# Kernel optimization log

Measured on AMD Instinct MI355X. Metric: run time of the kernel, lower is better.

Reference implementation:

```python
import jax, jax.numpy as jnp
import numpy as np


def _maxpool2x2(t):
    # t: [B, C, H, W] -> [B, C, H//2, W//2]
    B, C, H, W = t.shape
    return t.reshape(B, C, H // 2, 2, W // 2, 2).max(axis=(3, 5))


def setup_inputs() -> dict:
    key = jax.random.key(0)
    ks = jax.random.split(key, 6)
    ch = 64
    B, H, W = 16, 64, 64
    x = jax.random.normal(ks[0], (B, ch, H, W), dtype=jnp.float32)
    # 1x1 conv weights (spectral-norm wrapper just rescales weights; use unit-scale weights)
    w_theta = jax.random.normal(ks[1], (ch // 8, ch), dtype=jnp.float32) * 0.05
    w_phi = jax.random.normal(ks[2], (ch // 8, ch), dtype=jnp.float32) * 0.05
    w_g = jax.random.normal(ks[3], (ch // 2, ch), dtype=jnp.float32) * 0.05
    w_o = jax.random.normal(ks[4], (ch, ch // 2), dtype=jnp.float32) * 0.05
    gamma = jnp.float32(0.5)  # nonzero so attention branch contributes
    return {"x": x, "w_theta": w_theta, "w_phi": w_phi, "w_g": w_g, "w_o": w_o, "gamma": gamma}


def reference(x, w_theta, w_phi, w_g, w_o, gamma):
    B, C, H, W = x.shape
    N = H * W
    # 1x1 convs are channel contractions
    theta = jnp.einsum('oc,bchw->bohw', w_theta, x).reshape(B, -1, N)          # [B, C/8, N]
    phi = _maxpool2x2(jnp.einsum('oc,bchw->bohw', w_phi, x)).reshape(B, -1, N // 4)  # [B, C/8, N/4]
    g = _maxpool2x2(jnp.einsum('oc,bchw->bohw', w_g, x)).reshape(B, -1, N // 4)      # [B, C/2, N/4]
    # attention: no scaling (faithful to source)
    scores = jnp.einsum('bdn,bdm->bnm', theta, phi)       # [B, N, N/4]
    beta = jax.nn.softmax(scores, axis=-1)
    o = jnp.einsum('bdm,bnm->bdn', g, beta)               # [B, C/2, N]
    o = o.reshape(B, C // 2, H, W)
    o = jnp.einsum('oc,bchw->bohw', w_o, o)               # [B, C, H, W]
    return gamma * o + x
```

## Files before the change

kernel.cpp:

```cpp
#include <hip/hip_runtime.h>

#define BB 16
#define CC 64
#define NN 4096
#define MM 1024

typedef unsigned short u16;
typedef unsigned int u32;
typedef __attribute__((ext_vector_type(8))) short bf16x8;
typedef __attribute__((ext_vector_type(4))) float f32x4;

__device__ inline u16 f2bf(float f) {
    union { float f; u32 u; } v; v.f = f;
    return (u16)((v.u + 0x7FFFu + ((v.u >> 16) & 1u)) >> 16);
}
__device__ inline bf16x8 ld_bf16x8(const u16* p) {
    union { uint4 u; bf16x8 b; } c; c.u = *(const uint4*)p; return c.b;
}
__device__ inline bf16x8 ld2_bf16x8(const u16* p0, const u16* p1) {
    union { uint2 u[2]; bf16x8 b; } c;
    c.u[0] = *(const uint2*)p0;
    c.u[1] = *(const uint2*)p1;
    return c.b;
}
__device__ inline uint2 pack4(u16 a, u16 b, u16 c, u16 d) {
    uint2 r; r.x = (u32)a | ((u32)b << 16); r.y = (u32)c | ((u32)d << 16); return r;
}


__global__ __launch_bounds__(256) void prep_kernel(
    const float* __restrict__ x, const float* __restrict__ w_theta,
    const float* __restrict__ w_phi, const float* __restrict__ w_g,
    u16* __restrict__ theta_b, u16* __restrict__ phi_b, u16* __restrict__ gT_b)
{
    __shared__ float wT[64 * 48];

    const int t = threadIdx.x, w = t >> 6, l = t & 63;
    const int b = blockIdx.y;

    for (int i = t; i < 64 * 8; i += 256)  { int o = i >> 6, c = i & 63; wT[c * 48 + o] = w_theta[i]; }
    for (int i = t; i < 64 * 8; i += 256)  { int o = i >> 6, c = i & 63; wT[c * 48 + 8 + o] = w_phi[i]; }
    for (int i = t; i < 64 * 32; i += 256) { int o = i >> 6, c = i & 63; wT[c * 48 + 16 + o] = w_g[i]; }
    __syncthreads();

    const int nbase = blockIdx.x * 256;
    const float* xb = x + (size_t)b * CC * NN + nbase + 4 * l;

    float acc[12][4];
    #pragma unroll
    for (int k = 0; k < 12; ++k)
        #pragma unroll
        for (int p = 0; p < 4; ++p) acc[k][p] = 0.f;

    #pragma unroll 4
    for (int c = 0; c < 64; ++c) {
        const float4 xv = *(const float4*)(xb + c * NN);
        const float4* wp = (const float4*)(wT + c * 48 + w * 12);
        const float4 wa = wp[0], wb = wp[1], wc = wp[2];
        const float wk[12] = {wa.x, wa.y, wa.z, wa.w, wb.x, wb.y, wb.z, wb.w,
                              wc.x, wc.y, wc.z, wc.w};
        #pragma unroll
        for (int k = 0; k < 12; ++k) {
            acc[k][0] += wk[k] * xv.x; acc[k][1] += wk[k] * xv.y;
            acc[k][2] += wk[k] * xv.z; acc[k][3] += wk[k] * xv.w;
        }
    }

    if (w == 0) {
        #pragma unroll
        for (int p = 0; p < 4; ++p) {
            union { u16 s[8]; uint4 v; } tb;
            #pragma unroll
            for (int k = 0; k < 8; ++k) tb.s[k] = f2bf(acc[k][p]);
            *(uint4*)(theta_b + ((size_t)b * NN + nbase + 4 * l + p) * 8) = tb.v;
        }
    }

    const int start = (w == 0) ? 8 : 0;
    float v0[12], v1[12];
    #pragma unroll
    for (int k = 0; k < 12; ++k) {
        if (k < start) continue;
        float h0 = fmaxf(acc[k][0], acc[k][1]);
        float h1 = fmaxf(acc[k][2], acc[k][3]);
        v0[k] = fmaxf(h0, __shfl_xor(h0, 16, 64));
        v1[k] = fmaxf(h1, __shfl_xor(h1, 16, 64));
    }
    if ((l & 16) == 0) {
        const int prow = l >> 5;
        const int m = (blockIdx.x * 2 + prow) * 32 + 2 * (l & 15);
        #pragma unroll
        for (int k = 0; k < 12; ++k) {
            if (k < start) continue;
            const int kg = w * 12 + k;
            if (kg < 16) {
                phi_b[((size_t)b * MM + m) * 8 + (kg - 8)]     = f2bf(v0[k]);
                phi_b[((size_t)b * MM + m + 1) * 8 + (kg - 8)] = f2bf(v1[k]);
            } else {
                *(u32*)(gT_b + (size_t)b * 32 * MM + (size_t)(kg - 16) * MM + m) =
                    (u32)f2bf(v0[k]) | ((u32)f2bf(v1[k]) << 16);
            }
        }
    }
}

__global__ __launch_bounds__(256, 4) void attn_out_kernel(
    const u16* __restrict__ theta_b, const u16* __restrict__ phi_b,
    const u16* __restrict__ gT_b, const float* __restrict__ w_o,
    const float* __restrict__ x, const float* __restrict__ gamma_p,
    float* __restrict__ out)
{
    __shared__ u16 gs[32 * 136];
    __shared__ u16 oS[64 * 40];

    const int t = threadIdx.x, w = t >> 6, lane = t & 63;
    const int m16 = lane & 15, quad = lane >> 4;
    const int b = blockIdx.y, qbase = blockIdx.x * 64;

    bf16x8 thB = {0, 0, 0, 0, 0, 0, 0, 0};
    if (quad == 0)
        thB = ld_bf16x8(theta_b + ((size_t)b * NN + qbase + w * 16 + m16) * 8);

    bf16x8 woA[4];
    #pragma unroll
    for (int cf = 0; cf < 4; ++cf) {
        const float* wp = w_o + (cf * 16 + m16) * 32 + quad * 8;
        const float4 f0 = *(const float4*)wp;
        const float4 f1 = *(const float4*)(wp + 4);
        bf16x8 a;
        a[0] = f2bf(f0.x); a[1] = f2bf(f0.y); a[2] = f2bf(f0.z); a[3] = f2bf(f0.w);
        a[4] = f2bf(f1.x); a[5] = f2bf(f1.y); a[6] = f2bf(f1.z); a[7] = f2bf(f1.w);
        woA[cf] = a;
    }

    bf16x8 onesA;
    #pragma unroll
    for (int i = 0; i < 8; ++i) onesA[i] = (short)0x3F80;

    const f32x4 zero4 = {0.f, 0.f, 0.f, 0.f};
    f32x4 oT0 = zero4, oT1 = zero4, lacc = zero4;

    const u16* phg = phi_b + (size_t)b * MM * 8;
    const u16* gtg = gT_b + (size_t)b * 32 * MM;

    for (int it = 0; it < 8; ++it) {
        const int keybase = it * 128;
        __syncthreads();
        #pragma unroll
        for (int p2 = 0; p2 < 2; ++p2) {
            const int d = p2 * 16 + (t >> 4);
            const int k0 = (t & 15) * 8;
            *(uint4*)(gs + d * 136 + k0) =
                *(const uint4*)(gtg + (size_t)d * MM + keybase + k0);
        }
        __syncthreads();

        #pragma unroll
        for (int kblk = 0; kblk < 4; ++kblk) {
            bf16x8 phA0 = {0, 0, 0, 0, 0, 0, 0, 0};
            bf16x8 phA1 = {0, 0, 0, 0, 0, 0, 0, 0};
            if (quad == 0) {
                phA0 = ld_bf16x8(phg + (size_t)(keybase + kblk * 32 + m16) * 8);
                phA1 = ld_bf16x8(phg + (size_t)(keybase + kblk * 32 + 16 + m16) * 8);
            }
            const f32x4 Sa = __builtin_amdgcn_mfma_f32_16x16x32_bf16(phA0, thB, zero4, 0, 0, 0);
            const f32x4 Sb = __builtin_amdgcn_mfma_f32_16x16x32_bf16(phA1, thB, zero4, 0, 0, 0);

            bf16x8 pB;
            #pragma unroll
            for (int r = 0; r < 4; ++r) {
                pB[r]     = (short)f2bf(__expf(Sa[r]));
                pB[4 + r] = (short)f2bf(__expf(Sb[r]));
            }

            const u16* g0p = gs + m16 * 136 + kblk * 32 + quad * 4;
            const u16* g1p = gs + (16 + m16) * 136 + kblk * 32 + quad * 4;
            const bf16x8 gA0 = ld2_bf16x8(g0p, g0p + 16);
            const bf16x8 gA1 = ld2_bf16x8(g1p, g1p + 16);

            oT0  = __builtin_amdgcn_mfma_f32_16x16x32_bf16(gA0, pB, oT0, 0, 0, 0);
            oT1  = __builtin_amdgcn_mfma_f32_16x16x32_bf16(gA1, pB, oT1, 0, 0, 0);
            lacc = __builtin_amdgcn_mfma_f32_16x16x32_bf16(onesA, pB, lacc, 0, 0, 0);
        }
    }

    const float inv = 1.0f / lacc[0];
    u16* orow = oS + (w * 16 + m16) * 40;
    *(uint2*)(orow + quad * 4) =
        pack4(f2bf(oT0[0] * inv), f2bf(oT0[1] * inv), f2bf(oT0[2] * inv), f2bf(oT0[3] * inv));
    *(uint2*)(orow + 16 + quad * 4) =
        pack4(f2bf(oT1[0] * inv), f2bf(oT1[1] * inv), f2bf(oT1[2] * inv), f2bf(oT1[3] * inv));
    __syncthreads();

    const bf16x8 oB = ld_bf16x8(oS + (w * 16 + m16) * 40 + quad * 8);
    const float gamma = *gamma_p;
    #pragma unroll
    for (int cf = 0; cf < 4; ++cf) {
        const f32x4 D = __builtin_amdgcn_mfma_f32_16x16x32_bf16(woA[cf], oB, zero4, 0, 0, 0);
        #pragma unroll
        for (int r = 0; r < 4; ++r) {
            const int c = cf * 16 + quad * 4 + r;
            const size_t adr = ((size_t)b * CC + c) * NN + qbase + w * 16 + m16;
            out[adr] = gamma * D[r] + x[adr];
        }
    }
}

extern "C" void kernel_launch(void* const* d_in, const int* in_sizes, int n_in,
                              void* d_out, int out_size, void* d_ws, size_t ws_size,
                              hipStream_t stream) {
    const float* x       = (const float*)d_in[0];
    const float* w_theta = (const float*)d_in[1];
    const float* w_phi   = (const float*)d_in[2];
    const float* w_g     = (const float*)d_in[3];
    const float* w_o     = (const float*)d_in[4];
    const float* gamma   = (const float*)d_in[5];

    u16* theta_b = (u16*)d_ws;
    u16* phi_b   = theta_b + 524288;
    u16* gT_b    = phi_b + 131072;
    float* out   = (float*)d_out;

    prep_kernel<<<dim3(16, 16), 256, 0, stream>>>(x, w_theta, w_phi, w_g,
                                                  theta_b, phi_b, gT_b);
    attn_out_kernel<<<dim3(64, 16), 256, 0, stream>>>(theta_b, phi_b, gT_b,
                                                      w_o, x, gamma, out);
}
```

Before: 120.2 us.

## Restructure prep projection and stage phi/g in LDS with register prefetch

The prep kernel now assigns one pixel per thread and reads weights directly from global memory, computing all 48 output channels. It performs the 2x2 max-pool through a lane shuffle plus an LDS staging buffer instead of the earlier shuffle-only scheme. In the attention kernel, all of phi for the batch is copied into LDS once, and g is processed in 256-key chunks with a register prefetch of the next chunk, halving the number of barriers. Softmax and output bf16 conversion now use the packed bf16 conversion intrinsic. The trade-offs are higher LDS use per block, which may lower occupancy, and more register pressure in prep.

```diff
diff --git a/kernel.cpp b/kernel.cpp
--- a/kernel.cpp
+++ b/kernel.cpp
@@ -1,4 +1,5 @@
 #include <hip/hip_runtime.h>
+#include <hip/hip_bf16.h>
 
 #define BB 16
 #define CC 64
@@ -23,8 +24,9 @@
     c.u[1] = *(const uint2*)p1;
     return c.b;
 }
-__device__ inline uint2 pack4(u16 a, u16 b, u16 c, u16 d) {
-    uint2 r; r.x = (u32)a | ((u32)b << 16); r.y = (u32)c | ((u32)d << 16); return r;
+__device__ inline u32 cvt_pk_bf16(float lo, float hi) {
+    __hip_bfloat162 h = __float22bfloat162_rn(make_float2(lo, hi));
+    return *(u32*)&h;
 }
 
 
@@ -33,74 +35,69 @@
     const float* __restrict__ w_phi, const float* __restrict__ w_g,
     u16* __restrict__ theta_b, u16* __restrict__ phi_b, u16* __restrict__ gT_b)
 {
-    __shared__ float wT[64 * 48];
-
-    const int t = threadIdx.x, w = t >> 6, l = t & 63;
+    __shared__ float pool[40 * 128];
+
+    const int t = threadIdx.x;
     const int b = blockIdx.y;
-
-    for (int i = t; i < 64 * 8; i += 256)  { int o = i >> 6, c = i & 63; wT[c * 48 + o] = w_theta[i]; }
-    for (int i = t; i < 64 * 8; i += 256)  { int o = i >> 6, c = i & 63; wT[c * 48 + 8 + o] = w_phi[i]; }
-    for (int i = t; i < 64 * 32; i += 256) { int o = i >> 6, c = i & 63; wT[c * 48 + 16 + o] = w_g[i]; }
+    const int nbase = blockIdx.x * 256;
+    const int p = nbase + t;
+    const float* xb = x + (size_t)b * CC * NN + p;
+
+    float acc[48];
+    #pragma unroll
+    for (int k = 0; k < 48; ++k) acc[k] = 0.f;
+
+    #pragma unroll 2
+    for (int c4 = 0; c4 < 64; c4 += 4) {
+        const float x0 = xb[(size_t)(c4 + 0) * NN];
+        const float x1 = xb[(size_t)(c4 + 1) * NN];
+        const float x2 = xb[(size_t)(c4 + 2) * NN];
+        const float x3 = xb[(size_t)(c4 + 3) * NN];
+        #pragma unroll
+        for (int k = 0; k < 8; ++k) {
+            const float4 wv = *(const float4*)(w_theta + k * 64 + c4);
+            acc[k] += wv.x * x0 + wv.y * x1 + wv.z * x2 + wv.w * x3;
+        }
+        #pragma unroll
+        for (int k = 0; k < 8; ++k) {
+            const float4 wv = *(const float4*)(w_phi + k * 64 + c4);
+            acc[8 + k] += wv.x * x0 + wv.y * x1 + wv.z * x2 + wv.w * x3;
+        }
+        #pragma unroll
+        for (int k = 0; k < 32; ++k) {
+            const float4 wv = *(const float4*)(w_g + k * 64 + c4);
+            acc[16 + k] += wv.x * x0 + wv.y * x1 + wv.z * x2 + wv.w * x3;
+        }
+    }
+
+    {
+        union { u16 s[8]; uint4 v; } tb;
+        #pragma unroll
+        for (int k = 0; k < 8; ++k) tb.s[k] = f2bf(acc[k]);
+        *(uint4*)(theta_b + ((size_t)b * NN + p) * 8) = tb.v;
+    }
+
+    const int row = t >> 6, col = t & 63;
+    float hv[40];
+    #pragma unroll
+    for (int k = 0; k < 40; ++k) {
+        const float v = acc[8 + k];
+        hv[k] = fmaxf(v, __shfl_xor(v, 1, 64));
+    }
+    if ((col & 1) == 0) {
+        const int pc = col >> 1;
+        #pragma unroll
+        for (int k = 0; k < 40; ++k) pool[k * 128 + row * 32 + pc] = hv[k];
+    }
     __syncthreads();
 
-    const int nbase = blockIdx.x * 256;
-    const float* xb = x + (size_t)b * CC * NN + nbase + 4 * l;
-
-    float acc[12][4];
-    #pragma unroll
-    for (int k = 0; k < 12; ++k)
-        #pragma unroll
-        for (int p = 0; p < 4; ++p) acc[k][p] = 0.f;
-
-    #pragma unroll 4
-    for (int c = 0; c < 64; ++c) {
-        const float4 xv = *(const float4*)(xb + c * NN);
-        const float4* wp = (const float4*)(wT + c * 48 + w * 12);
-        const float4 wa = wp[0], wb = wp[1], wc = wp[2];
-        const float wk[12] = {wa.x, wa.y, wa.z, wa.w, wb.x, wb.y, wb.z, wb.w,
-                              wc.x, wc.y, wc.z, wc.w};
-        #pragma unroll
-        for (int k = 0; k < 12; ++k) {
-            acc[k][0] += wk[k] * xv.x; acc[k][1] += wk[k] * xv.y;
-            acc[k][2] += wk[k] * xv.z; acc[k][3] += wk[k] * xv.w;
-        }
-    }
-
-    if (w == 0) {
-        #pragma unroll
-        for (int p = 0; p < 4; ++p) {
-            union { u16 s[8]; uint4 v; } tb;
-            #pragma unroll
-            for (int k = 0; k < 8; ++k) tb.s[k] = f2bf(acc[k][p]);
-            *(uint4*)(theta_b + ((size_t)b * NN + nbase + 4 * l + p) * 8) = tb.v;
-        }
-    }
-
-    const int start = (w == 0) ? 8 : 0;
-    float v0[12], v1[12];
-    #pragma unroll
-    for (int k = 0; k < 12; ++k) {
-        if (k < start) continue;
-        float h0 = fmaxf(acc[k][0], acc[k][1]);
-        float h1 = fmaxf(acc[k][2], acc[k][3]);
-        v0[k] = fmaxf(h0, __shfl_xor(h0, 16, 64));
-        v1[k] = fmaxf(h1, __shfl_xor(h1, 16, 64));
-    }
-    if ((l & 16) == 0) {
-        const int prow = l >> 5;
-        const int m = (blockIdx.x * 2 + prow) * 32 + 2 * (l & 15);
-        #pragma unroll
-        for (int k = 0; k < 12; ++k) {
-            if (k < start) continue;
-            const int kg = w * 12 + k;
-            if (kg < 16) {
-                phi_b[((size_t)b * MM + m) * 8 + (kg - 8)]     = f2bf(v0[k]);
-                phi_b[((size_t)b * MM + m + 1) * 8 + (kg - 8)] = f2bf(v1[k]);
-            } else {
-                *(u32*)(gT_b + (size_t)b * 32 * MM + (size_t)(kg - 16) * MM + m) =
-                    (u32)f2bf(v0[k]) | ((u32)f2bf(v1[k]) << 16);
-            }
-        }
+    for (int i = t; i < 2560; i += 256) {
+        const int k = i >> 6, rem = i & 63, rp = rem >> 5, pcol = rem & 31;
+        const float v = fmaxf(pool[k * 128 + (2 * rp) * 32 + pcol],
+                              pool[k * 128 + (2 * rp + 1) * 32 + pcol]);
+        const int m = (blockIdx.x * 2 + rp) * 32 + pcol;
+        if (k < 8) phi_b[((size_t)b * MM + m) * 8 + k] = f2bf(v);
+        else       gT_b[(size_t)b * 32 * MM + (size_t)(k - 8) * MM + m] = f2bf(v);
     }
 }
 
@@ -110,12 +107,20 @@
     const float* __restrict__ x, const float* __restrict__ gamma_p,
     float* __restrict__ out)
 {
-    __shared__ u16 gs[32 * 136];
+    __shared__ u16 phis[1024 * 8];
+    __shared__ u16 gs[32 * 264];
     __shared__ u16 oS[64 * 40];
 
     const int t = threadIdx.x, w = t >> 6, lane = t & 63;
     const int m16 = lane & 15, quad = lane >> 4;
     const int b = blockIdx.y, qbase = blockIdx.x * 64;
+
+    const u16* phg = phi_b + (size_t)b * MM * 8;
+    const u16* gtg = gT_b + (size_t)b * 32 * MM;
+
+    #pragma unroll
+    for (int i = 0; i < 4; ++i)
+        ((uint4*)phis)[i * 256 + t] = ((const uint4*)phg)[i * 256 + t];
 
     bf16x8 thB = {0, 0, 0, 0, 0, 0, 0, 0};
     if (quad == 0)
@@ -140,56 +145,69 @@
     const f32x4 zero4 = {0.f, 0.f, 0.f, 0.f};
     f32x4 oT0 = zero4, oT1 = zero4, lacc = zero4;
 
-    const u16* phg = phi_b + (size_t)b * MM * 8;
-    const u16* gtg = gT_b + (size_t)b * 32 * MM;
-
-    for (int it = 0; it < 8; ++it) {
-        const int keybase = it * 128;
+    uint4 r[4];
+    #pragma unroll
+    for (int i = 0; i < 4; ++i) {
+        const int f = i * 256 + t, d = f >> 5, ku = f & 31;
+        r[i] = *(const uint4*)(gtg + (size_t)d * MM + ku * 8);
+    }
+
+    for (int c = 0; c < 4; ++c) {
         __syncthreads();
         #pragma unroll
-        for (int p2 = 0; p2 < 2; ++p2) {
-            const int d = p2 * 16 + (t >> 4);
-            const int k0 = (t & 15) * 8;
-            *(uint4*)(gs + d * 136 + k0) =
-                *(const uint4*)(gtg + (size_t)d * MM + keybase + k0);
+        for (int i = 0; i < 4; ++i) {
+            const int f = i * 256 + t, d = f >> 5, ku = f & 31;
+            *(uint4*)(gs + d * 264 + ku * 8) = r[i];
         }
         __syncthreads();
-
-        #pragma unroll
-        for (int kblk = 0; kblk < 4; ++kblk) {
+        if (c < 3) {
+            #pragma unroll
+            for (int i = 0; i < 4; ++i) {
+                const int f = i * 256 + t, d = f >> 5, ku = f & 31;
+                r[i] = *(const uint4*)(gtg + (size_t)d * MM + (c + 1) * 256 + ku * 8);
+            }
+        }
+
+        #pragma unroll
+        for (int kblk = 0; kblk < 8; ++kblk) {
+            const int kb = c * 256 + kblk * 32;
             bf16x8 phA0 = {0, 0, 0, 0, 0, 0, 0, 0};
             bf16x8 phA1 = {0, 0, 0, 0, 0, 0, 0, 0};
             if (quad == 0) {
-                phA0 = ld_bf16x8(phg + (size_t)(keybase + kblk * 32 + m16) * 8);
-                phA1 = ld_bf16x8(phg + (size_t)(keybase + kblk * 32 + 16 + m16) * 8);
+                phA0 = ld_bf16x8(phis + (size_t)(kb + m16) * 8);
+                phA1 = ld_bf16x8(phis + (size_t)(kb + 16 + m16) * 8);
             }
             const f32x4 Sa = __builtin_amdgcn_mfma_f32_16x16x32_bf16(phA0, thB, zero4, 0, 0, 0);
             const f32x4 Sb = __builtin_amdgcn_mfma_f32_16x16x32_bf16(phA1, thB, zero4, 0, 0, 0);
 
-            bf16x8 pB;
-            #pragma unroll
-            for (int r = 0; r < 4; ++r) {
-                pB[r]     = (short)f2bf(__expf(Sa[r]));
-                pB[4 + r] = (short)f2bf(__expf(Sb[r]));
-            }
-
-            const u16* g0p = gs + m16 * 136 + kblk * 32 + quad * 4;
-            const u16* g1p = gs + (16 + m16) * 136 + kblk * 32 + quad * 4;
+            union { u32 d[4]; bf16x8 v; } pb;
+            pb.d[0] = cvt_pk_bf16(__expf(Sa[0]), __expf(Sa[1]));
+            pb.d[1] = cvt_pk_bf16(__expf(Sa[2]), __expf(Sa[3]));
+            pb.d[2] = cvt_pk_bf16(__expf(Sb[0]), __expf(Sb[1]));
+            pb.d[3] = cvt_pk_bf16(__expf(Sb[2]), __expf(Sb[3]));
+
+            const u16* g0p = gs + m16 * 264 + kblk * 32 + quad * 4;
+            const u16* g1p = gs + (16 + m16) * 264 + kblk * 32 + quad * 4;
             const bf16x8 gA0 = ld2_bf16x8(g0p, g0p + 16);
             const bf16x8 gA1 = ld2_bf16x8(g1p, g1p + 16);
 
-            oT0  = __builtin_amdgcn_mfma_f32_16x16x32_bf16(gA0, pB, oT0, 0, 0, 0);
-            oT1  = __builtin_amdgcn_mfma_f32_16x16x32_bf16(gA1, pB, oT1, 0, 0, 0);
-            lacc = __builtin_amdgcn_mfma_f32_16x16x32_bf16(onesA, pB, lacc, 0, 0, 0);
+            oT0  = __builtin_amdgcn_mfma_f32_16x16x32_bf16(gA0, pb.v, oT0, 0, 0, 0);
+            oT1  = __builtin_amdgcn_mfma_f32_16x16x32_bf16(gA1, pb.v, oT1, 0, 0, 0);
+            lacc = __builtin_amdgcn_mfma_f32_16x16x32_bf16(onesA, pb.v, lacc, 0, 0, 0);
         }
     }
 
     const float inv = 1.0f / lacc[0];
     u16* orow = oS + (w * 16 + m16) * 40;
-    *(uint2*)(orow + quad * 4) =
-        pack4(f2bf(oT0[0] * inv), f2bf(oT0[1] * inv), f2bf(oT0[2] * inv), f2bf(oT0[3] * inv));
-    *(uint2*)(orow + 16 + quad * 4) =
-        pack4(f2bf(oT1[0] * inv), f2bf(oT1[1] * inv), f2bf(oT1[2] * inv), f2bf(oT1[3] * inv));
+    {
+        uint2 a, b2;
+        a.x  = cvt_pk_bf16(oT0[0] * inv, oT0[1] * inv);
+        a.y  = cvt_pk_bf16(oT0[2] * inv, oT0[3] * inv);
+        b2.x = cvt_pk_bf16(oT1[0] * inv, oT1[1] * inv);
+        b2.y = cvt_pk_bf16(oT1[2] * inv, oT1[3] * inv);
+        *(uint2*)(orow + quad * 4) = a;
+        *(uint2*)(orow + 16 + quad * 4) = b2;
+    }
     __syncthreads();
 
     const bf16x8 oB = ld_bf16x8(oS + (w * 16 + m16) * 40 + quad * 8);
@@ -198,10 +216,10 @@
     for (int cf = 0; cf < 4; ++cf) {
         const f32x4 D = __builtin_amdgcn_mfma_f32_16x16x32_bf16(woA[cf], oB, zero4, 0, 0, 0);
         #pragma unroll
-        for (int r = 0; r < 4; ++r) {
-            const int c = cf * 16 + quad * 4 + r;
-            const size_t adr = ((size_t)b * CC + c) * NN + qbase + w * 16 + m16;
-            out[adr] = gamma * D[r] + x[adr];
+        for (int rr = 0; rr < 4; ++rr) {
+            const int cch = cf * 16 + quad * 4 + rr;
+            const size_t adr = ((size_t)b * CC + cch) * NN + qbase + w * 16 + m16;
+            out[adr] = gamma * D[rr] + x[adr];
         }
     }
 }
```

Result: slower. 165.2 us (+37.4%).
